# Kernel optimization log

Measured on AMD Instinct MI355X. Metric: run time of the kernel, lower is better.

## Reference

```python
import jax, jax.numpy as jnp
import numpy as np

ALPHA = 0.2  # LeakyReLU negative slope


def setup_inputs() -> dict:
    key = jax.random.key(0)
    ks = jax.random.split(key, 7)
    N, D, O, R = 50000, 128, 128, 64
    E1, E2 = 800000, 200000
    return {
        "input": jax.random.normal(ks[0], (N, D), jnp.float32),
        "edge": jax.random.randint(ks[1], (2, E1), 0, N),
        "edge_embed": jax.random.normal(ks[2], (E1, R), jnp.float32),
        "edge_list_nhop": jax.random.randint(ks[3], (2, E2), 0, N),
        "edge_embed_nhop": jax.random.normal(ks[4], (E2, R), jnp.float32),
        "a": jax.random.normal(ks[5], (O, 2 * D + R), jnp.float32) * 0.05,
        "a_2": jax.random.normal(ks[6], (1, O), jnp.float32) * 0.05,
    }


def _gat_forward(x, edge, e_embed, a, a_2):
    N, D = x.shape
    src, dst = edge[0], edge[1]
    # a @ [x_src; x_dst; e_embed]^T computed blockwise (avoids [E, 2D+R] concat)
    a_src, a_dst, a_rel = a[:, :D], a[:, D:2 * D], a[:, 2 * D:]
    edge_m = x[src] @ a_src.T + x[dst] @ a_dst.T + e_embed @ a_rel.T  # [E, O] == edge_m^T
    score = edge_m @ a_2[0]                                            # [E]
    powers = -jnp.where(score > 0, score, ALPHA * score)               # -LeakyReLU
    edge_e = jnp.exp(powers)                                           # [E]
    e_rowsum = jax.ops.segment_sum(edge_e, src, num_segments=N)[:, None]  # [N, 1]
    e_rowsum = jnp.where(e_rowsum == 0.0, 1e-12, e_rowsum)
    edge_w = edge_e[:, None] * edge_m                                  # [E, O]
    h_prime = jax.ops.segment_sum(edge_w, src, num_segments=N)         # [N, O]
    h_prime = h_prime / e_rowsum
    return jax.nn.elu(h_prime)  # concat=True path


def reference(input, edge, edge_embed, edge_list_nhop, edge_embed_nhop, a, a_2):
    edge_all = jnp.concatenate([edge, edge_list_nhop], axis=1)        # [2, E1+E2]
    embed_all = jnp.concatenate([edge_embed, edge_embed_nhop], axis=0)  # [E1+E2, R]
    return _gat_forward(input, edge_all, embed_all, a, a_2)
```

## Files before the change

kernel.cpp:

```cpp
#include <hip/hip_runtime.h>
#include <hip/hip_bf16.h>

#define LRELU_ALPHA 0.2f

typedef __bf16 bf16x8 __attribute__((ext_vector_type(8)));
typedef float f32x4 __attribute__((ext_vector_type(4)));

__device__ __forceinline__ float waveReduceSum(float v) {
#pragma unroll
    for (int off = 32; off > 0; off >>= 1)
        v += __shfl_xor(v, off, 64);
    return v;
}

__global__ void k_prep(const float* __restrict__ a, const float* __restrict__ a2,
                       float* __restrict__ vall, __hip_bfloat16* __restrict__ ABf) {
    int idx = blockIdx.x * 256 + threadIdx.x;
    if (idx < 128 * 320) ABf[idx] = __float2bfloat16(a[idx]);
    if (idx < 320) {
        float s = 0.f;
#pragma unroll 8
        for (int o = 0; o < 128; ++o) s += a[o * 320 + idx] * a2[o];
        vall[idx] = s;
    }
}

__global__ void k_node_scores(const float* __restrict__ x, const float* __restrict__ vall,
                              float* __restrict__ s_src, float* __restrict__ s_dst, int N) {
    int wid = (int)((blockIdx.x * (size_t)blockDim.x + threadIdx.x) >> 6);
    int lane = threadIdx.x & 63;
    if (wid >= N) return;
    const float* xp = x + (size_t)wid * 128;
    float x0 = xp[lane], x1 = xp[lane + 64];
    float ps = x0 * vall[lane] + x1 * vall[lane + 64];
    float pd = x0 * vall[128 + lane] + x1 * vall[192 + lane];
    ps = waveReduceSum(ps);
    pd = waveReduceSum(pd);
    if (lane == 0) { s_src[wid] = ps; s_dst[wid] = pd; }
}

__global__ void k_escore(const int* __restrict__ e1, int E1,
                         const int* __restrict__ e2, int E2,
                         const float* __restrict__ emb1, const float* __restrict__ emb2,
                         const float* __restrict__ vall,
                         const float* __restrict__ s_src, const float* __restrict__ s_dst,
                         float* __restrict__ ee, int* __restrict__ cnt) {
    int gid = blockIdx.x * blockDim.x + threadIdx.x;
    int wave = gid >> 6;
    int lane = threadIdx.x & 63;
    int g = lane >> 4, s = lane & 15;
    int e = wave * 4 + g;
    int E = E1 + E2;
    if (e >= E) return;
    const float* ep = (e < E1) ? emb1 + (size_t)e * 64 : emb2 + (size_t)(e - E1) * 64;
    float4 v = *reinterpret_cast<const float4*>(ep + s * 4);
    float4 r = *reinterpret_cast<const float4*>(vall + 256 + s * 4);
    float d = v.x * r.x + v.y * r.y + v.z * r.z + v.w * r.w;
    d += __shfl_xor(d, 1, 64);
    d += __shfl_xor(d, 2, 64);
    d += __shfl_xor(d, 4, 64);
    d += __shfl_xor(d, 8, 64);
    if (s == 0) {
        int src, dst;
        if (e < E1) { src = e1[e]; dst = e1[E1 + e]; }
        else { int t = e - E1; src = e2[t]; dst = e2[E2 + t]; }
        float score = s_src[src] + s_dst[dst] + d;
        float pz = score > 0.f ? score : LRELU_ALPHA * score;
        ee[e] = __expf(-pz);
        atomicAdd(&cnt[src], 1);
    }
}

__global__ void k_scan1(const int* __restrict__ cnt, int* __restrict__ bsum, int N) {
    __shared__ int red[256];
    int t = threadIdx.x;
    int idx = blockIdx.x * 256 + t;
    red[t] = (idx < N) ? cnt[idx] : 0;
    __syncthreads();
    for (int off = 128; off > 0; off >>= 1) {
        if (t < off) red[t] += red[t + off];
        __syncthreads();
    }
    if (t == 0) bsum[blockIdx.x] = red[0];
}

__global__ void k_scan2(int* __restrict__ bsum, int nb) {
    __shared__ int tmp[256];
    int t = threadIdx.x;
    int v = (t < nb) ? bsum[t] : 0;
    tmp[t] = v;
    __syncthreads();
    for (int off = 1; off < 256; off <<= 1) {
        int add = (t >= off) ? tmp[t - off] : 0;
        __syncthreads();
        tmp[t] += add;
        __syncthreads();
    }
    if (t < nb) bsum[t] = tmp[t] - v;
}

__global__ void k_scan3(const int* __restrict__ cnt, const int* __restrict__ bsum,
                        int* __restrict__ start, int* __restrict__ cursor, int N, int E) {
    __shared__ int tmp[256];
    int t = threadIdx.x;
    int idx = blockIdx.x * 256 + t;
    int v = (idx < N) ? cnt[idx] : 0;
    tmp[t] = v;
    __syncthreads();
    for (int off = 1; off < 256; off <<= 1) {
        int add = (t >= off) ? tmp[t - off] : 0;
        __syncthreads();
        tmp[t] += add;
        __syncthreads();
    }
    if (idx < N) {
        int excl = tmp[t] - v + bsum[blockIdx.x];
        start[idx] = excl;
        cursor[idx] = excl;
    }
    if (blockIdx.x == 0 && t == 0) start[N] = E;
}

__global__ void k_scatter(const int* __restrict__ e1, int E1, const int* __restrict__ e2, int E2,
                          int* __restrict__ cursor, int2* __restrict__ se) {
    int e = blockIdx.x * blockDim.x + threadIdx.x;
    if (e >= E1 + E2) return;
    int src, dst;
    if (e < E1) { src = e1[e]; dst = e1[E1 + e]; }
    else { int t = e - E1; src = e2[t]; dst = e2[E2 + t]; }
    int p = atomicAdd(&cursor[src], 1);
    se[p] = make_int2(dst, e);
}

__global__ void k_gather(const float* __restrict__ x,
                         const float* __restrict__ emb1, const float* __restrict__ emb2, int E1,
                         const int* __restrict__ start, const int2* __restrict__ se,
                         const float* __restrict__ eetab,
                         __hip_bfloat16* __restrict__ G, float* __restrict__ sxf, int N) {
    int n = (int)((blockIdx.x * (size_t)blockDim.x + threadIdx.x) >> 6);
    int lane = threadIdx.x & 63;
    if (n >= N) return;
    n = __builtin_amdgcn_readfirstlane(n);
    int b = start[n], en = start[n + 1];
    float ux = 0.f, uy = 0.f, w0 = 0.f, rs = 0.f;
    int p = b;
    for (; p + 3 < en; p += 4) {
        int2 d0 = se[p], d1 = se[p + 1], d2 = se[p + 2], d3 = se[p + 3];
        float e0 = eetab[d0.y], e1v = eetab[d1.y], e2v = eetab[d2.y], e3v = eetab[d3.y];
        const float* ep0 = (d0.y < E1) ? emb1 + (size_t)d0.y * 64 : emb2 + (size_t)(d0.y - E1) * 64;
        const float* ep1 = (d1.y < E1) ? emb1 + (size_t)d1.y * 64 : emb2 + (size_t)(d1.y - E1) * 64;
        const float* ep2 = (d2.y < E1) ? emb1 + (size_t)d2.y * 64 : emb2 + (size_t)(d2.y - E1) * 64;
        const float* ep3 = (d3.y < E1) ? emb1 + (size_t)d3.y * 64 : emb2 + (size_t)(d3.y - E1) * 64;
        float2 xv0 = *reinterpret_cast<const float2*>(x + (size_t)d0.x * 128 + 2 * lane);
        float2 xv1 = *reinterpret_cast<const float2*>(x + (size_t)d1.x * 128 + 2 * lane);
        float2 xv2 = *reinterpret_cast<const float2*>(x + (size_t)d2.x * 128 + 2 * lane);
        float2 xv3 = *reinterpret_cast<const float2*>(x + (size_t)d3.x * 128 + 2 * lane);
        float em0 = ep0[lane], em1 = ep1[lane], em2 = ep2[lane], em3 = ep3[lane];
        ux += e0 * xv0.x; uy += e0 * xv0.y; w0 += e0 * em0; rs += e0;
        ux += e1v * xv1.x; uy += e1v * xv1.y; w0 += e1v * em1; rs += e1v;
        ux += e2v * xv2.x; uy += e2v * xv2.y; w0 += e2v * em2; rs += e2v;
        ux += e3v * xv3.x; uy += e3v * xv3.y; w0 += e3v * em3; rs += e3v;
    }
    for (; p < en; ++p) {
        int2 d0 = se[p];
        float e0 = eetab[d0.y];
        const float* ep0 = (d0.y < E1) ? emb1 + (size_t)d0.y * 64 : emb2 + (size_t)(d0.y - E1) * 64;
        float2 xv0 = *reinterpret_cast<const float2*>(x + (size_t)d0.x * 128 + 2 * lane);
        ux += e0 * xv0.x; uy += e0 * xv0.y; w0 += e0 * ep0[lane]; rs += e0;
    }
    float inv = (rs == 0.f) ? 0.f : 1.f / rs;
    __hip_bfloat16* gp = G + (size_t)n * 192;
    __hip_bfloat162 uv;
    uv.x = __float2bfloat16(ux * inv);
    uv.y = __float2bfloat16(uy * inv);
    *reinterpret_cast<__hip_bfloat162*>(gp + 2 * lane) = uv;
    gp[128 + lane] = __float2bfloat16(w0 * inv);
    if (lane == 0) sxf[n] = (rs == 0.f) ? 0.f : 1.f;
}

__global__ __launch_bounds__(256) void k_mfma(
    const float* __restrict__ x, const __hip_bfloat16* __restrict__ G,
    const __hip_bfloat16* __restrict__ ABf, const float* __restrict__ sxf,
    float* __restrict__ out, int N) {
    int lane = threadIdx.x & 63;
    int wave = threadIdx.x >> 6;
    int m0 = blockIdx.x * 64 + wave * 16;
    int q = lane >> 4, m = lane & 15;
    int rowm = m0 + m; if (rowm >= N) rowm = N - 1;
    const float* xr = x + (size_t)rowm * 128 + q * 8;
    const __hip_bfloat16* gr = G + (size_t)rowm * 192 + q * 8;
    const __hip_bfloat16* br = ABf + (size_t)m * 320 + q * 8;
    f32x4 acc[8];
#pragma unroll
    for (int c = 0; c < 8; ++c) acc[c] = f32x4{0.f, 0.f, 0.f, 0.f};

#pragma unroll
    for (int s = 0; s < 4; ++s) {
        float4 xa = *reinterpret_cast<const float4*>(xr + s * 32);
        float4 xb = *reinterpret_cast<const float4*>(xr + s * 32 + 4);
        bf16x8 af;
        af[0] = (__bf16)xa.x; af[1] = (__bf16)xa.y; af[2] = (__bf16)xa.z; af[3] = (__bf16)xa.w;
        af[4] = (__bf16)xb.x; af[5] = (__bf16)xb.y; af[6] = (__bf16)xb.z; af[7] = (__bf16)xb.w;
#pragma unroll
        for (int c = 0; c < 8; ++c) {
            bf16x8 bf = *reinterpret_cast<const bf16x8*>(br + (size_t)c * 16 * 320 + s * 32);
            acc[c] = __builtin_amdgcn_mfma_f32_16x16x32_bf16(af, bf, acc[c], 0, 0, 0);
        }
    }
#pragma unroll
    for (int s = 0; s < 6; ++s) {
        bf16x8 af = *reinterpret_cast<const bf16x8*>(gr + s * 32);
#pragma unroll
        for (int c = 0; c < 8; ++c) {
            bf16x8 bf = *reinterpret_cast<const bf16x8*>(br + (size_t)c * 16 * 320 + 128 + s * 32);
            acc[c] = __builtin_amdgcn_mfma_f32_16x16x32_bf16(af, bf, acc[c], 0, 0, 0);
        }
    }

    float sxr[4];
#pragma unroll
    for (int r = 0; r < 4; ++r) {
        int n = m0 + q * 4 + r;
        sxr[r] = (n < N) ? sxf[n] : 0.f;
    }
#pragma unroll
    for (int c = 0; c < 8; ++c) {
#pragma unroll
        for (int r = 0; r < 4; ++r) {
            int n = m0 + q * 4 + r;
            if (n < N) {
                float h = acc[c][r] * sxr[r];
                out[(size_t)n * 128 + c * 16 + m] = h > 0.f ? h : __expf(h) - 1.f;
            }
        }
    }
}

extern "C" void kernel_launch(void* const* d_in, const int* in_sizes, int n_in,
                              void* d_out, int out_size, void* d_ws, size_t ws_size,
                              hipStream_t stream) {
    const float* x    = (const float*)d_in[0];
    const int*   e1   = (const int*)d_in[1];
    const float* emb1 = (const float*)d_in[2];
    const int*   e2   = (const int*)d_in[3];
    const float* emb2 = (const float*)d_in[4];
    const float* a    = (const float*)d_in[5];
    const float* a2   = (const float*)d_in[6];
    float* out = (float*)d_out;

    const int N  = in_sizes[0] / 128;
    const int E1 = in_sizes[1] / 2;
    const int E2 = in_sizes[3] / 2;
    const int E  = E1 + E2;
    const int NB = (N + 255) / 256;

    float* ws    = (float*)d_ws;
    float* vall  = ws;
    __hip_bfloat16* ABf = (__hip_bfloat16*)(ws + 512);
    float* s_src = ws + 512 + 20480;
    float* s_dst = s_src + N;
    float* sxf   = s_dst + N;
    int*   cnt    = (int*)(sxf + N);
    int*   bsum   = cnt + N;
    int*   start  = bsum + 256;
    int*   cursor = start + N + 1;
    float* ee     = (float*)(cursor + N + 1);
    if ((size_t)(ee - ws) & 1) ee += 1;
    int2*  se     = (int2*)(ee + E);
    size_t go = (size_t)((char*)(se + E) - (char*)d_ws);
    go = (go + 15) & ~(size_t)15;
    __hip_bfloat16* G = (__hip_bfloat16*)((char*)d_ws + go);

    size_t needed = go + (size_t)N * 192 * sizeof(__hip_bfloat16);
    if (ws_size < needed) return;

    hipMemsetAsync(cnt, 0, (size_t)N * sizeof(int), stream);

    k_prep<<<(128 * 320 + 255) / 256, 256, 0, stream>>>(a, a2, vall, ABf);
    k_node_scores<<<(N * 64 + 255) / 256, 256, 0, stream>>>(x, vall, s_src, s_dst, N);
    {
        long long waves = ((long long)E + 3) / 4;
        long long blocks = (waves * 64 + 255) / 256;
        k_escore<<<(int)blocks, 256, 0, stream>>>(e1, E1, e2, E2, emb1, emb2,
                                                  vall, s_src, s_dst, ee, cnt);
    }
    k_scan1<<<NB, 256, 0, stream>>>(cnt, bsum, N);
    k_scan2<<<1, 256, 0, stream>>>(bsum, NB);
    k_scan3<<<NB, 256, 0, stream>>>(cnt, bsum, start, cursor, N, E);
    k_scatter<<<(E + 255) / 256, 256, 0, stream>>>(e1, E1, e2, E2, cursor, se);
    k_gather<<<(N * 64 + 255) / 256, 256, 0, stream>>>(
        x, emb1, emb2, E1, start, se, ee, G, sxf, N);
    k_mfma<<<(N + 63) / 64, 256, 0, stream>>>(x, G, ABf, sxf, out, N);
}
```

Baseline: 608.2 us.

## Fuse edge score computation into gather and gather x as bf16

Drops the separate per-edge score kernel. The exp(-LeakyReLU) attention weight is now recomputed inside the per-node gather, reusing the edge embedding row that the gather already loads, with a wave reduction per edge. That removes one full pass over the 1M×64 embedding array and the ee buffer. A bf16 copy of x is written during node scoring, so the gather reads half the bytes per neighbour row and the MFMA kernel loads bf16 directly instead of converting. The costs are a 64-lane shuffle reduction per edge inside the gather loop, a lower unroll (2 instead of 4, so less memory-level parallelism), and bf16 rounding of x in the aggregation.

```diff
diff --git a/kernel.cpp b/kernel.cpp
--- a/kernel.cpp
+++ b/kernel.cpp
@@ -26,12 +26,15 @@
 }
 
 __global__ void k_node_scores(const float* __restrict__ x, const float* __restrict__ vall,
-                              float* __restrict__ s_src, float* __restrict__ s_dst, int N) {
+                              float* __restrict__ s_src, float* __restrict__ s_dst,
+                              __hip_bfloat16* __restrict__ XBf, int N) {
     int wid = (int)((blockIdx.x * (size_t)blockDim.x + threadIdx.x) >> 6);
     int lane = threadIdx.x & 63;
     if (wid >= N) return;
     const float* xp = x + (size_t)wid * 128;
     float x0 = xp[lane], x1 = xp[lane + 64];
+    XBf[(size_t)wid * 128 + lane]      = __float2bfloat16(x0);
+    XBf[(size_t)wid * 128 + 64 + lane] = __float2bfloat16(x1);
     float ps = x0 * vall[lane] + x1 * vall[lane + 64];
     float pd = x0 * vall[128 + lane] + x1 * vall[192 + lane];
     ps = waveReduceSum(ps);
@@ -39,36 +42,12 @@
     if (lane == 0) { s_src[wid] = ps; s_dst[wid] = pd; }
 }
 
-__global__ void k_escore(const int* __restrict__ e1, int E1,
-                         const int* __restrict__ e2, int E2,
-                         const float* __restrict__ emb1, const float* __restrict__ emb2,
-                         const float* __restrict__ vall,
-                         const float* __restrict__ s_src, const float* __restrict__ s_dst,
-                         float* __restrict__ ee, int* __restrict__ cnt) {
-    int gid = blockIdx.x * blockDim.x + threadIdx.x;
-    int wave = gid >> 6;
-    int lane = threadIdx.x & 63;
-    int g = lane >> 4, s = lane & 15;
-    int e = wave * 4 + g;
-    int E = E1 + E2;
-    if (e >= E) return;
-    const float* ep = (e < E1) ? emb1 + (size_t)e * 64 : emb2 + (size_t)(e - E1) * 64;
-    float4 v = *reinterpret_cast<const float4*>(ep + s * 4);
-    float4 r = *reinterpret_cast<const float4*>(vall + 256 + s * 4);
-    float d = v.x * r.x + v.y * r.y + v.z * r.z + v.w * r.w;
-    d += __shfl_xor(d, 1, 64);
-    d += __shfl_xor(d, 2, 64);
-    d += __shfl_xor(d, 4, 64);
-    d += __shfl_xor(d, 8, 64);
-    if (s == 0) {
-        int src, dst;
-        if (e < E1) { src = e1[e]; dst = e1[E1 + e]; }
-        else { int t = e - E1; src = e2[t]; dst = e2[E2 + t]; }
-        float score = s_src[src] + s_dst[dst] + d;
-        float pz = score > 0.f ? score : LRELU_ALPHA * score;
-        ee[e] = __expf(-pz);
-        atomicAdd(&cnt[src], 1);
-    }
+__global__ void k_count(const int* __restrict__ e1, int E1, const int* __restrict__ e2, int E2,
+                        int* __restrict__ cnt) {
+    int e = blockIdx.x * blockDim.x + threadIdx.x;
+    if (e >= E1 + E2) return;
+    int src = (e < E1) ? e1[e] : e2[e - E1];
+    atomicAdd(&cnt[src], 1);
 }
 
 __global__ void k_scan1(const int* __restrict__ cnt, int* __restrict__ bsum, int N) {
@@ -132,41 +111,57 @@
     se[p] = make_int2(dst, e);
 }
 
-__global__ void k_gather(const float* __restrict__ x,
+__global__ void k_gather(const __hip_bfloat16* __restrict__ XBf,
                          const float* __restrict__ emb1, const float* __restrict__ emb2, int E1,
                          const int* __restrict__ start, const int2* __restrict__ se,
-                         const float* __restrict__ eetab,
+                         const float* __restrict__ vall,
+                         const float* __restrict__ s_src, const float* __restrict__ s_dst,
                          __hip_bfloat16* __restrict__ G, float* __restrict__ sxf, int N) {
     int n = (int)((blockIdx.x * (size_t)blockDim.x + threadIdx.x) >> 6);
     int lane = threadIdx.x & 63;
     if (n >= N) return;
     n = __builtin_amdgcn_readfirstlane(n);
     int b = start[n], en = start[n + 1];
+    float r2l = vall[256 + lane];
+    float ssrc = s_src[n];
     float ux = 0.f, uy = 0.f, w0 = 0.f, rs = 0.f;
     int p = b;
-    for (; p + 3 < en; p += 4) {
-        int2 d0 = se[p], d1 = se[p + 1], d2 = se[p + 2], d3 = se[p + 3];
-        float e0 = eetab[d0.y], e1v = eetab[d1.y], e2v = eetab[d2.y], e3v = eetab[d3.y];
+    for (; p + 1 < en; p += 2) {
+        int2 d0 = se[p], d1 = se[p + 1];
         const float* ep0 = (d0.y < E1) ? emb1 + (size_t)d0.y * 64 : emb2 + (size_t)(d0.y - E1) * 64;
         const float* ep1 = (d1.y < E1) ? emb1 + (size_t)d1.y * 64 : emb2 + (size_t)(d1.y - E1) * 64;
-        const float* ep2 = (d2.y < E1) ? emb1 + (size_t)d2.y * 64 : emb2 + (size_t)(d2.y - E1) * 64;
-        const float* ep3 = (d3.y < E1) ? emb1 + (size_t)d3.y * 64 : emb2 + (size_t)(d3.y - E1) * 64;
-        float2 xv0 = *reinterpret_cast<const float2*>(x + (size_t)d0.x * 128 + 2 * lane);
-        float2 xv1 = *reinterpret_cast<const float2*>(x + (size_t)d1.x * 128 + 2 * lane);
-        float2 xv2 = *reinterpret_cast<const float2*>(x + (size_t)d2.x * 128 + 2 * lane);
-        float2 xv3 = *reinterpret_cast<const float2*>(x + (size_t)d3.x * 128 + 2 * lane);
-        float em0 = ep0[lane], em1 = ep1[lane], em2 = ep2[lane], em3 = ep3[lane];
-        ux += e0 * xv0.x; uy += e0 * xv0.y; w0 += e0 * em0; rs += e0;
-        ux += e1v * xv1.x; uy += e1v * xv1.y; w0 += e1v * em1; rs += e1v;
-        ux += e2v * xv2.x; uy += e2v * xv2.y; w0 += e2v * em2; rs += e2v;
-        ux += e3v * xv3.x; uy += e3v * xv3.y; w0 += e3v * em3; rs += e3v;
-    }
-    for (; p < en; ++p) {
+        float em0 = ep0[lane], em1 = ep1[lane];
+        __hip_bfloat162 xv0 = *reinterpret_cast<const __hip_bfloat162*>(XBf + (size_t)d0.x * 128 + 2 * lane);
+        __hip_bfloat162 xv1 = *reinterpret_cast<const __hip_bfloat162*>(XBf + (size_t)d1.x * 128 + 2 * lane);
+        float sd0 = s_dst[d0.x], sd1 = s_dst[d1.x];
+        float t0 = em0 * r2l, t1 = em1 * r2l;
+#pragma unroll
+        for (int off = 32; off > 0; off >>= 1) {
+            t0 += __shfl_xor(t0, off, 64);
+            t1 += __shfl_xor(t1, off, 64);
+        }
+        float sc0 = ssrc + sd0 + t0;
+        float sc1 = ssrc + sd1 + t1;
+        float pz0 = sc0 > 0.f ? sc0 : LRELU_ALPHA * sc0;
+        float pz1 = sc1 > 0.f ? sc1 : LRELU_ALPHA * sc1;
+        float e0 = __expf(-pz0), e1v = __expf(-pz1);
+        ux += e0 * __bfloat162float(xv0.x); uy += e0 * __bfloat162float(xv0.y);
+        w0 += e0 * em0; rs += e0;
+        ux += e1v * __bfloat162float(xv1.x); uy += e1v * __bfloat162float(xv1.y);
+        w0 += e1v * em1; rs += e1v;
+    }
+    if (p < en) {
         int2 d0 = se[p];
-        float e0 = eetab[d0.y];
         const float* ep0 = (d0.y < E1) ? emb1 + (size_t)d0.y * 64 : emb2 + (size_t)(d0.y - E1) * 64;
-        float2 xv0 = *reinterpret_cast<const float2*>(x + (size_t)d0.x * 128 + 2 * lane);
-        ux += e0 * xv0.x; uy += e0 * xv0.y; w0 += e0 * ep0[lane]; rs += e0;
+        float em0 = ep0[lane];
+        __hip_bfloat162 xv0 = *reinterpret_cast<const __hip_bfloat162*>(XBf + (size_t)d0.x * 128 + 2 * lane);
+        float sd0 = s_dst[d0.x];
+        float t0 = waveReduceSum(em0 * r2l);
+        float sc0 = ssrc + sd0 + t0;
+        float pz0 = sc0 > 0.f ? sc0 : LRELU_ALPHA * sc0;
+        float e0 = __expf(-pz0);
+        ux += e0 * __bfloat162float(xv0.x); uy += e0 * __bfloat162float(xv0.y);
+        w0 += e0 * em0; rs += e0;
     }
     float inv = (rs == 0.f) ? 0.f : 1.f / rs;
     __hip_bfloat16* gp = G + (size_t)n * 192;
@@ -179,7 +174,7 @@
 }
 
 __global__ __launch_bounds__(256) void k_mfma(
-    const float* __restrict__ x, const __hip_bfloat16* __restrict__ G,
+    const __hip_bfloat16* __restrict__ XBf, const __hip_bfloat16* __restrict__ G,
     const __hip_bfloat16* __restrict__ ABf, const float* __restrict__ sxf,
     float* __restrict__ out, int N) {
     int lane = threadIdx.x & 63;
@@ -187,7 +182,7 @@
     int m0 = blockIdx.x * 64 + wave * 16;
     int q = lane >> 4, m = lane & 15;
     int rowm = m0 + m; if (rowm >= N) rowm = N - 1;
-    const float* xr = x + (size_t)rowm * 128 + q * 8;
+    const __hip_bfloat16* xr = XBf + (size_t)rowm * 128 + q * 8;
     const __hip_bfloat16* gr = G + (size_t)rowm * 192 + q * 8;
     const __hip_bfloat16* br = ABf + (size_t)m * 320 + q * 8;
     f32x4 acc[8];
@@ -196,11 +191,7 @@
 
 #pragma unroll
     for (int s = 0; s < 4; ++s) {
-        float4 xa = *reinterpret_cast<const float4*>(xr + s * 32);
-        float4 xb = *reinterpret_cast<const float4*>(xr + s * 32 + 4);
-        bf16x8 af;
-        af[0] = (__bf16)xa.x; af[1] = (__bf16)xa.y; af[2] = (__bf16)xa.z; af[3] = (__bf16)xa.w;
-        af[4] = (__bf16)xb.x; af[5] = (__bf16)xb.y; af[6] = (__bf16)xb.z; af[7] = (__bf16)xb.w;
+        bf16x8 af = *reinterpret_cast<const bf16x8*>(xr + s * 32);
 #pragma unroll
         for (int c = 0; c < 8; ++c) {
             bf16x8 bf = *reinterpret_cast<const bf16x8*>(br + (size_t)c * 16 * 320 + s * 32);
@@ -264,10 +255,13 @@
     int*   bsum   = cnt + N;
     int*   start  = bsum + 256;
     int*   cursor = start + N + 1;
-    float* ee     = (float*)(cursor + N + 1);
-    if ((size_t)(ee - ws) & 1) ee += 1;
-    int2*  se     = (int2*)(ee + E);
-    size_t go = (size_t)((char*)(se + E) - (char*)d_ws);
+    size_t so = (size_t)((char*)(cursor + N + 1) - (char*)d_ws);
+    so = (so + 15) & ~(size_t)15;
+    int2*  se = (int2*)((char*)d_ws + so);
+    size_t xo = so + (size_t)E * sizeof(int2);
+    xo = (xo + 15) & ~(size_t)15;
+    __hip_bfloat16* XBf = (__hip_bfloat16*)((char*)d_ws + xo);
+    size_t go = xo + (size_t)N * 128 * sizeof(__hip_bfloat16);
     go = (go + 15) & ~(size_t)15;
     __hip_bfloat16* G = (__hip_bfloat16*)((char*)d_ws + go);
 
@@ -277,18 +271,13 @@
     hipMemsetAsync(cnt, 0, (size_t)N * sizeof(int), stream);
 
     k_prep<<<(128 * 320 + 255) / 256, 256, 0, stream>>>(a, a2, vall, ABf);
-    k_node_scores<<<(N * 64 + 255) / 256, 256, 0, stream>>>(x, vall, s_src, s_dst, N);
-    {
-        long long waves = ((long long)E + 3) / 4;
-        long long blocks = (waves * 64 + 255) / 256;
-        k_escore<<<(int)blocks, 256, 0, stream>>>(e1, E1, e2, E2, emb1, emb2,
-                                                  vall, s_src, s_dst, ee, cnt);
-    }
+    k_node_scores<<<(N * 64 + 255) / 256, 256, 0, stream>>>(x, vall, s_src, s_dst, XBf, N);
+    k_count<<<(E + 255) / 256, 256, 0, stream>>>(e1, E1, e2, E2, cnt);
     k_scan1<<<NB, 256, 0, stream>>>(cnt, bsum, N);
     k_scan2<<<1, 256, 0, stream>>>(bsum, NB);
     k_scan3<<<NB, 256, 0, stream>>>(cnt, bsum, start, cursor, N, E);
     k_scatter<<<(E + 255) / 256, 256, 0, stream>>>(e1, E1, e2, E2, cursor, se);
     k_gather<<<(N * 64 + 255) / 256, 256, 0, stream>>>(
-        x, emb1, emb2, E1, start, se, ee, G, sxf, N);
-    k_mfma<<<(N + 63) / 64, 256, 0, stream>>>(x, G, ABf, sxf, out, N);
-}
+        XBf, emb1, emb2, E1, start, se, vall, s_src, s_dst, G, sxf, N);
+    k_mfma<<<(N + 63) / 64, 256, 0, stream>>>(XBf, G, ABf, sxf, out, N);
+}
```

Result: faster. 565.2 us (-7.1%).
